# Kernel optimization log

Measured on AMD Instinct MI355X. Metric: run time of the kernel, lower is better.

## Reference

```python
import jax, jax.numpy as jnp
import numpy as np

EPS = 1e-8


def setup_inputs() -> dict:
    key = jax.random.key(0)
    kx, kw = jax.random.split(key)
    B, T, D_IN, D_OUT = 2, 2048, 4096, 16384
    x = jax.random.normal(kx, (B, T, D_IN), dtype=jnp.float32)
    # kaiming-uniform-ish scale for a (D_OUT, D_IN) linear weight
    bound = float(np.sqrt(6.0 / D_IN))
    weight = jax.random.uniform(kw, (D_OUT, D_IN), dtype=jnp.float32,
                                minval=-bound, maxval=bound)
    return {"x": x, "weight": weight}


def reference(x, weight):
    # --- ternary weight quantization (STE; value identical in train/eval) ---
    scale_w = jnp.mean(jnp.abs(weight))                       # scalar absmean
    w_q = jnp.clip(jnp.round(weight / (scale_w + EPS)), -1.0, 1.0) * scale_w
    w_quant = weight + jax.lax.stop_gradient(w_q - weight)    # STE

    # --- per-token INT8 activation quantization ---
    gamma = jnp.max(jnp.abs(x), axis=-1, keepdims=True)       # (B, T, 1)
    x_quant = jnp.clip(jnp.round(127.0 * x / (gamma + EPS)), -128.0, 127.0)
    scale_x = gamma / 127.0                                   # (B, T, 1)

    # --- GEMM + dequant epilogue ---
    out = jnp.einsum("btd,od->bto", x_quant, w_quant)         # (B, T, D_OUT)
    return out * scale_x
```

## Files before the change

kernel.cpp:

```cpp
#include <hip/hip_runtime.h>


#define M_ROWS 4096
#define K_DIM  4096
#define N_DIM  16384
#define W_ELEMS (N_DIM * K_DIM)
#define EPSF 1e-8f

using i32x4 = __attribute__((ext_vector_type(4))) int;


__global__ void k_abs_partial(const float4* __restrict__ w4,
                              double* __restrict__ part) {
    const int tid = threadIdx.x;
    int idx = blockIdx.x * 256 + tid;
    double s = 0.0;
    #pragma unroll 4
    for (int it = 0; it < 32; ++it) {
        float4 v = w4[idx + it * (2048 * 256)];
        s += (double)fabsf(v.x) + (double)fabsf(v.y)
           + (double)fabsf(v.z) + (double)fabsf(v.w);
    }
    __shared__ double red[256];
    red[tid] = s;
    __syncthreads();
    for (int o = 128; o > 0; o >>= 1) {
        if (tid < o) red[tid] += red[tid + o];
        __syncthreads();
    }
    if (tid == 0) part[blockIdx.x] = red[0];
}

__global__ void k_abs_final(const double* __restrict__ part,
                            float* __restrict__ scales) {
    const int tid = threadIdx.x;
    double s = 0.0;
    #pragma unroll
    for (int k = 0; k < 8; ++k) s += part[tid + k * 256];
    __shared__ double red[256];
    red[tid] = s;
    __syncthreads();
    for (int o = 128; o > 0; o >>= 1) {
        if (tid < o) red[tid] += red[tid + o];
        __syncthreads();
    }
    if (tid == 0) {
        float sw = (float)(red[0] / (double)W_ELEMS);
        scales[0] = sw;
        scales[1] = sw + EPSF;
    }
}

__global__ void k_wquant(const float4* __restrict__ w4,
                         const float* __restrict__ scales,
                         char4* __restrict__ wq4) {
    const float seps = scales[1];
    int idx = blockIdx.x * 256 + threadIdx.x;
    const int stride = 8192 * 256;
    #pragma unroll
    for (int it = 0; it < 8; ++it) {
        int i = idx + it * stride;
        float4 v = w4[i];
        char4 q;
        q.x = (signed char)(int)fminf(fmaxf(rintf(v.x / seps), -1.0f), 1.0f);
        q.y = (signed char)(int)fminf(fmaxf(rintf(v.y / seps), -1.0f), 1.0f);
        q.z = (signed char)(int)fminf(fmaxf(rintf(v.z / seps), -1.0f), 1.0f);
        q.w = (signed char)(int)fminf(fmaxf(rintf(v.w / seps), -1.0f), 1.0f);
        wq4[i] = q;
    }
}

__global__ void k_xquant(const float4* __restrict__ x4,
                         char4* __restrict__ xq4,
                         float* __restrict__ sx) {
    const int row = blockIdx.x, tid = threadIdx.x;
    const float4* xr = x4 + (size_t)row * (K_DIM / 4);
    float4 v[4];
    float m = 0.0f;
    #pragma unroll
    for (int j = 0; j < 4; ++j) {
        v[j] = xr[tid + j * 256];
        m = fmaxf(m, fmaxf(fmaxf(fabsf(v[j].x), fabsf(v[j].y)),
                           fmaxf(fabsf(v[j].z), fabsf(v[j].w))));
    }
    __shared__ float red[256];
    red[tid] = m;
    __syncthreads();
    for (int o = 128; o > 0; o >>= 1) {
        if (tid < o) red[tid] = fmaxf(red[tid], red[tid + o]);
        __syncthreads();
    }
    const float gamma = red[0];
    const float ge = gamma + EPSF;
    char4* out = xq4 + (size_t)row * (K_DIM / 4);
    #pragma unroll
    for (int j = 0; j < 4; ++j) {
        char4 q;
        q.x = (signed char)(int)fminf(fmaxf(rintf(127.0f * v[j].x / ge), -128.0f), 127.0f);
        q.y = (signed char)(int)fminf(fmaxf(rintf(127.0f * v[j].y / ge), -128.0f), 127.0f);
        q.z = (signed char)(int)fminf(fmaxf(rintf(127.0f * v[j].z / ge), -128.0f), 127.0f);
        q.w = (signed char)(int)fminf(fmaxf(rintf(127.0f * v[j].w / ge), -128.0f), 127.0f);
        out[tid + j * 256] = q;
    }
    if (tid == 0) sx[row] = gamma / 127.0f;
}

__device__ __forceinline__ void gload16(const signed char* g, const signed char* l) {
    __builtin_amdgcn_global_load_lds(
        (const __attribute__((address_space(1))) void*)g,
        (__attribute__((address_space(3))) void*)l, 16, 0, 0);
}

__global__ __launch_bounds__(256)
void k_gemm(const signed char* __restrict__ Aq,
            const signed char* __restrict__ Bq,
            const float* __restrict__ sx,
            const float* __restrict__ scales,
            float* __restrict__ C) {
    __shared__ __align__(16) signed char sA[128 * 64];
    __shared__ __align__(16) signed char sB[128 * 64];

    const int tid  = threadIdx.x;
    const int lane = tid & 63;
    const int wid  = tid >> 6;

    const int nwg = gridDim.x;
    const int cpx = nwg >> 3;
    const int bid = blockIdx.x;
    const int wg  = (bid & 7) * cpx + (bid >> 3);
    const int num_n = N_DIM / 128;
    const int per_group = 8 * num_n;
    const int gidx   = wg / per_group;
    const int within = wg - gidx * per_group;
    const int pm = gidx * 8 + (within & 7);
    const int pn = within >> 3;

    int prow[2], pcol[2], ldsoff[2];
    #pragma unroll
    for (int i = 0; i < 2; ++i) {
        int p = i * 4096 + tid * 16;
        int r = p >> 6;
        int j = (p >> 4) & 3;
        int js = j ^ ((r >> 1) & 3);
        prow[i]  = r;
        pcol[i]  = js << 4;
        ldsoff[i] = i * 4096 + wid * 1024;
    }
    const signed char* aSrc0 = Aq + (size_t)(pm * 128 + prow[0]) * K_DIM + pcol[0];
    const signed char* aSrc1 = Aq + (size_t)(pm * 128 + prow[1]) * K_DIM + pcol[1];
    const signed char* bSrc0 = Bq + (size_t)(pn * 128 + prow[0]) * K_DIM + pcol[0];
    const signed char* bSrc1 = Bq + (size_t)(pn * 128 + prow[1]) * K_DIM + pcol[1];

    const int wm  = (wid >> 1) * 64;
    const int wn  = (wid & 1) * 64;
    const int l15 = lane & 15;
    const int chunk = ((lane >> 4) ^ ((l15 >> 1) & 3)) << 4;

    i32x4 acc[4][4];
    #pragma unroll
    for (int a = 0; a < 4; ++a)
        #pragma unroll
        for (int b = 0; b < 4; ++b)
            acc[a][b] = (i32x4){0, 0, 0, 0};

    for (int kt = 0; kt < K_DIM / 64; ++kt) {
        const int ko = kt * 64;
        gload16(aSrc0 + ko, sA + ldsoff[0]);
        gload16(aSrc1 + ko, sA + ldsoff[1]);
        gload16(bSrc0 + ko, sB + ldsoff[0]);
        gload16(bSrc1 + ko, sB + ldsoff[1]);
        __syncthreads();

        i32x4 af[4], bf[4];
        #pragma unroll
        for (int f = 0; f < 4; ++f) {
            af[f] = *(const i32x4*)(sA + (wm + f * 16 + l15) * 64 + chunk);
            bf[f] = *(const i32x4*)(sB + (wn + f * 16 + l15) * 64 + chunk);
        }
        #pragma unroll
        for (int fm = 0; fm < 4; ++fm)
            #pragma unroll
            for (int fn = 0; fn < 4; ++fn)
                acc[fm][fn] = __builtin_amdgcn_mfma_i32_16x16x64_i8(
                    af[fm], bf[fn], acc[fm][fn], 0, 0, 0);
        __syncthreads();
    }

    const float sw = scales[0];
    const int gn0 = pn * 128 + wn + l15;
    const int gm_base = pm * 128 + wm + (lane >> 4) * 4;
    #pragma unroll
    for (int fm = 0; fm < 4; ++fm) {
        #pragma unroll
        for (int r = 0; r < 4; ++r) {
            const int gm = gm_base + fm * 16 + r;
            const float s = sx[gm] * sw;
            float* crow = C + (size_t)gm * N_DIM + gn0;
            #pragma unroll
            for (int fn = 0; fn < 4; ++fn)
                crow[fn * 16] = (float)acc[fm][fn][r] * s;
        }
    }
}

extern "C" void kernel_launch(void* const* d_in, const int* in_sizes, int n_in,
                              void* d_out, int out_size, void* d_ws, size_t ws_size,
                              hipStream_t stream) {
    const float* x = (const float*)d_in[0];
    const float* w = (const float*)d_in[1];
    float* out = (float*)d_out;
    char* ws = (char*)d_ws;

    float*  scales = (float*)(ws);
    double* part   = (double*)(ws + 1024);
    float*  sx     = (float*)(ws + 32 * 1024);
    signed char* xq = (signed char*)(ws + 64 * 1024);
    signed char* wq = xq + (size_t)M_ROWS * K_DIM;

    k_abs_partial<<<2048, 256, 0, stream>>>((const float4*)w, part);
    k_abs_final<<<1, 256, 0, stream>>>(part, scales);
    k_wquant<<<8192, 256, 0, stream>>>((const float4*)w, scales, (char4*)wq);
    k_xquant<<<M_ROWS, 256, 0, stream>>>((const float4*)x, (char4*)xq, sx);
    k_gemm<<<(M_ROWS / 128) * (N_DIM / 128), 256, 0, stream>>>(xq, wq, sx, scales, out);
}
```

Measured before the change: 500.4 us.

## Rewrite int8 GEMM as 256x256 tile, 8-wave, double-buffered pipelined kernel

Replaces the 128x128 single-buffered int8 MFMA GEMM with a 256x256 tile, 512-thread (8-wave) kernel that uses 128 KB of LDS as two buffers with K-step 128. Global-to-LDS loads for later K tiles are issued in quarter slices and interleaved with MFMA phases, using explicit vmcnt waits, barriers and raised wave priority around the math. An XOR swizzle avoids LDS bank conflicts. The aim is to hide global load latency and raise arithmetic intensity, at the cost of more registers (128 accumulators per thread) and a hand-tuned barrier schedule that is fragile to get right.

```diff
diff --git a/kernel.cpp b/kernel.cpp
--- a/kernel.cpp
+++ b/kernel.cpp
@@ -105,100 +105,151 @@
     if (tid == 0) sx[row] = gamma / 127.0f;
 }
 
-__device__ __forceinline__ void gload16(const signed char* g, const signed char* l) {
+__device__ __forceinline__ void gload16(const signed char* g, signed char* l) {
     __builtin_amdgcn_global_load_lds(
         (const __attribute__((address_space(1))) void*)g,
         (__attribute__((address_space(3))) void*)l, 16, 0, 0);
 }
 
-__global__ __launch_bounds__(256)
-void k_gemm(const signed char* __restrict__ Aq,
-            const signed char* __restrict__ Bq,
-            const float* __restrict__ sx,
-            const float* __restrict__ scales,
-            float* __restrict__ C) {
-    __shared__ __align__(16) signed char sA[128 * 64];
-    __shared__ __align__(16) signed char sB[128 * 64];
+#define BAR()   __builtin_amdgcn_s_barrier()
+#define LGKM0() asm volatile("s_waitcnt lgkmcnt(0)" ::: "memory")
+#define VM6()   asm volatile("s_waitcnt vmcnt(6)" ::: "memory")
+#define PRIO1() __builtin_amdgcn_s_setprio(1)
+#define PRIO0() __builtin_amdgcn_s_setprio(0)
+
+__global__ __launch_bounds__(512, 2)
+void k_gemm8(const signed char* __restrict__ Aq,
+             const signed char* __restrict__ Bq,
+             const float* __restrict__ sx,
+             const float* __restrict__ scales,
+             float* __restrict__ C) {
+    __shared__ __align__(16) signed char lds[131072];
 
     const int tid  = threadIdx.x;
     const int lane = tid & 63;
     const int wid  = tid >> 6;
-
-    const int nwg = gridDim.x;
-    const int cpx = nwg >> 3;
+    const int l15  = lane & 15;
+    const int qg   = lane >> 4;
+    const int swz  = l15 & 7;
+
     const int bid = blockIdx.x;
-    const int wg  = (bid & 7) * cpx + (bid >> 3);
-    const int num_n = N_DIM / 128;
-    const int per_group = 8 * num_n;
-    const int gidx   = wg / per_group;
-    const int within = wg - gidx * per_group;
+    const int wg  = (bid & 7) * 128 + (bid >> 3);
+    const int gidx   = wg >> 9;
+    const int within = wg & 511;
     const int pm = gidx * 8 + (within & 7);
     const int pn = within >> 3;
 
-    int prow[2], pcol[2], ldsoff[2];
-    #pragma unroll
-    for (int i = 0; i < 2; ++i) {
-        int p = i * 4096 + tid * 16;
-        int r = p >> 6;
-        int j = (p >> 4) & 3;
-        int js = j ^ ((r >> 1) & 3);
-        prow[i]  = r;
-        pcol[i]  = js << 4;
-        ldsoff[i] = i * 4096 + wid * 1024;
-    }
-    const signed char* aSrc0 = Aq + (size_t)(pm * 128 + prow[0]) * K_DIM + pcol[0];
-    const signed char* aSrc1 = Aq + (size_t)(pm * 128 + prow[1]) * K_DIM + pcol[1];
-    const signed char* bSrc0 = Bq + (size_t)(pn * 128 + prow[0]) * K_DIM + pcol[0];
-    const signed char* bSrc1 = Bq + (size_t)(pn * 128 + prow[1]) * K_DIM + pcol[1];
-
-    const int wm  = (wid >> 1) * 64;
-    const int wn  = (wid & 1) * 64;
-    const int l15 = lane & 15;
-    const int chunk = ((lane >> 4) ^ ((l15 >> 1) & 3)) << 4;
-
-    i32x4 acc[4][4];
-    #pragma unroll
-    for (int a = 0; a < 4; ++a)
+    const int wm = (wid >> 2) * 128;
+    const int wn = (wid & 3) * 64;
+
+    const int l3 = lane >> 3, l7 = lane & 7;
+    const int lane_off = l3 * K_DIM + ((l7 ^ l3) << 4);
+    const signed char* Asrc = Aq + (size_t)(pm * 256) * K_DIM + lane_off;
+    const signed char* Bsrc = Bq + (size_t)(pn * 256) * K_DIM + lane_off;
+    const int ar0 = wid * 8;
+    const int br0 = (wid >> 2) * 64 + (wid & 3) * 8;
+
+    auto stageA = [&](int buf, int mh, int kt) {
+        const int r0 = mh * 64 + ar0;
+        const signed char* s = Asrc + (size_t)r0 * K_DIM + kt * 128;
+        signed char* d = lds + buf * 65536 + r0 * 128;
+        gload16(s, d);
+        gload16(s + (size_t)128 * K_DIM, d + 128 * 128);
+    };
+    auto stageB = [&](int buf, int nh, int kt) {
+        const int r0 = nh * 32 + br0;
+        const signed char* s = Bsrc + (size_t)r0 * K_DIM + kt * 128;
+        signed char* d = lds + buf * 65536 + 32768 + r0 * 128;
+        gload16(s, d);
+        gload16(s + (size_t)128 * K_DIM, d + 128 * 128);
+    };
+
+    i32x4 acc[8][4];
+    #pragma unroll
+    for (int a = 0; a < 8; ++a)
         #pragma unroll
         for (int b = 0; b < 4; ++b)
             acc[a][b] = (i32x4){0, 0, 0, 0};
 
-    for (int kt = 0; kt < K_DIM / 64; ++kt) {
-        const int ko = kt * 64;
-        gload16(aSrc0 + ko, sA + ldsoff[0]);
-        gload16(aSrc1 + ko, sA + ldsoff[1]);
-        gload16(bSrc0 + ko, sB + ldsoff[0]);
-        gload16(bSrc1 + ko, sB + ldsoff[1]);
-        __syncthreads();
-
-        i32x4 af[4], bf[4];
-        #pragma unroll
-        for (int f = 0; f < 4; ++f) {
-            af[f] = *(const i32x4*)(sA + (wm + f * 16 + l15) * 64 + chunk);
-            bf[f] = *(const i32x4*)(sB + (wn + f * 16 + l15) * 64 + chunk);
+    i32x4 af[8], bf[4];
+    auto ldA = [&](int buf, int mh) {
+        const signed char* base = lds + buf * 65536;
+        #pragma unroll
+        for (int fm = 0; fm < 4; ++fm) {
+            const int ro = (wm + mh * 64 + fm * 16 + l15) * 128;
+            #pragma unroll
+            for (int ks = 0; ks < 2; ++ks)
+                af[fm * 2 + ks] = *(const i32x4*)(base + ro + (((ks * 4 + qg) ^ swz) << 4));
         }
-        #pragma unroll
-        for (int fm = 0; fm < 4; ++fm)
-            #pragma unroll
-            for (int fn = 0; fn < 4; ++fn)
-                acc[fm][fn] = __builtin_amdgcn_mfma_i32_16x16x64_i8(
-                    af[fm], bf[fn], acc[fm][fn], 0, 0, 0);
-        __syncthreads();
-    }
+    };
+    auto ldB = [&](int buf, int nh) {
+        const signed char* base = lds + buf * 65536 + 32768;
+        #pragma unroll
+        for (int fn = 0; fn < 2; ++fn) {
+            const int ro = (wn + nh * 32 + fn * 16 + l15) * 128;
+            #pragma unroll
+            for (int ks = 0; ks < 2; ++ks)
+                bf[fn * 2 + ks] = *(const i32x4*)(base + ro + (((ks * 4 + qg) ^ swz) << 4));
+        }
+    };
+    auto mma = [&](int mh, int nh) {
+        #pragma unroll
+        for (int ks = 0; ks < 2; ++ks)
+            #pragma unroll
+            for (int fm = 0; fm < 4; ++fm)
+                #pragma unroll
+                for (int fn = 0; fn < 2; ++fn)
+                    acc[mh * 4 + fm][nh * 2 + fn] = __builtin_amdgcn_mfma_i32_16x16x64_i8(
+                        af[fm * 2 + ks], bf[fn * 2 + ks], acc[mh * 4 + fm][nh * 2 + fn], 0, 0, 0);
+    };
+
+    stageA(0, 0, 0); stageB(0, 1, 0); stageA(0, 1, 0); stageB(0, 0, 0);
+    stageA(1, 0, 1); stageB(1, 1, 1); stageA(1, 1, 1);
+    VM6();
+    BAR();
+
+    for (int t = 0; t < 16; ++t) {
+        const int k1 = 2 * t + 1;
+        const int k2 = (2 * t + 2) & 31;
+        const int k3 = (2 * t + 3) & 31;
+
+        ldA(0, 0); ldB(0, 0); stageB(1, 0, k1);
+        BAR(); LGKM0(); PRIO1(); mma(0, 0); PRIO0(); BAR();
+        ldB(0, 1); stageA(0, 0, k2);
+        BAR(); LGKM0(); PRIO1(); mma(0, 1); PRIO0(); BAR();
+        ldA(0, 1); stageB(0, 1, k2);
+        BAR(); LGKM0(); PRIO1(); mma(1, 1); PRIO0(); BAR();
+        ldB(0, 0); stageA(0, 1, k2);
+        BAR(); LGKM0(); PRIO1(); mma(1, 0); PRIO0();
+        VM6();
+        BAR();
+        ldA(1, 0); ldB(1, 0); stageB(0, 0, k2);
+        BAR(); LGKM0(); PRIO1(); mma(0, 0); PRIO0(); BAR();
+        ldB(1, 1); stageA(1, 0, k3);
+        BAR(); LGKM0(); PRIO1(); mma(0, 1); PRIO0(); BAR();
+        ldA(1, 1); stageB(1, 1, k3);
+        BAR(); LGKM0(); PRIO1(); mma(1, 1); PRIO0(); BAR();
+        ldB(1, 0); stageA(1, 1, k3);
+        BAR(); LGKM0(); PRIO1(); mma(1, 0); PRIO0();
+        VM6();
+        BAR();
+    }
+    asm volatile("s_waitcnt vmcnt(0)" ::: "memory");
 
     const float sw = scales[0];
-    const int gn0 = pn * 128 + wn + l15;
-    const int gm_base = pm * 128 + wm + (lane >> 4) * 4;
-    #pragma unroll
-    for (int fm = 0; fm < 4; ++fm) {
+    const int gn0 = pn * 256 + wn + l15;
+    const int rb  = (lane >> 4) * 4;
+    #pragma unroll
+    for (int mi = 0; mi < 8; ++mi) {
+        const int rowoff = (mi >> 2) * 64 + (mi & 3) * 16;
         #pragma unroll
         for (int r = 0; r < 4; ++r) {
-            const int gm = gm_base + fm * 16 + r;
+            const int gm = pm * 256 + wm + rowoff + rb + r;
             const float s = sx[gm] * sw;
             float* crow = C + (size_t)gm * N_DIM + gn0;
             #pragma unroll
-            for (int fn = 0; fn < 4; ++fn)
-                crow[fn * 16] = (float)acc[fm][fn][r] * s;
+            for (int ni = 0; ni < 4; ++ni)
+                crow[(ni >> 1) * 32 + (ni & 1) * 16] = (float)acc[mi][ni][r] * s;
         }
     }
 }
@@ -221,5 +272,5 @@
     k_abs_final<<<1, 256, 0, stream>>>(part, scales);
     k_wquant<<<8192, 256, 0, stream>>>((const float4*)w, scales, (char4*)wq);
     k_xquant<<<M_ROWS, 256, 0, stream>>>((const float4*)x, (char4*)xq, sx);
-    k_gemm<<<(M_ROWS / 128) * (N_DIM / 128), 256, 0, stream>>>(xq, wq, sx, scales, out);
-}
+    k_gemm8<<<(M_ROWS / 256) * (N_DIM / 256), 512, 0, stream>>>(xq, wq, sx, scales, out);
+}
```

Measured after the change: 402.9 us. 19.5% less time.

## Rewrite int8 GEMM as 256x128 tile, 8-wave double-buffered pipelined kernel

Applied to the files above, without the earlier changes.

Replaces the 128x128, 4-wave GEMM with a 256x128 tile handled by 8 waves. It double-buffers LDS and splits each k-step into half-phases. Global-to-LDS loads for the next tiles are interleaved with MFMA work using s_waitcnt vmcnt(1), raw barriers, setprio and sched_barrier, and a new XOR swizzle layout is applied. The goal is to hide global load latency and cut per-k-step synchronisation stalls, at the cost of more LDS (48KB) and a delicate hand-written barrier schedule.

```diff
diff --git a/kernel.cpp b/kernel.cpp
--- a/kernel.cpp
+++ b/kernel.cpp
@@ -8,7 +8,6 @@
 #define EPSF 1e-8f
 
 using i32x4 = __attribute__((ext_vector_type(4))) int;
-
 
 __global__ void k_abs_partial(const float4* __restrict__ w4,
                               double* __restrict__ part) {
@@ -105,56 +104,58 @@
     if (tid == 0) sx[row] = gamma / 127.0f;
 }
 
-__device__ __forceinline__ void gload16(const signed char* g, const signed char* l) {
+__device__ __forceinline__ void gload16(const signed char* g, signed char* l) {
     __builtin_amdgcn_global_load_lds(
         (const __attribute__((address_space(1))) void*)g,
         (__attribute__((address_space(3))) void*)l, 16, 0, 0);
 }
 
-__global__ __launch_bounds__(256)
-void k_gemm(const signed char* __restrict__ Aq,
-            const signed char* __restrict__ Bq,
-            const float* __restrict__ sx,
-            const float* __restrict__ scales,
-            float* __restrict__ C) {
-    __shared__ __align__(16) signed char sA[128 * 64];
-    __shared__ __align__(16) signed char sB[128 * 64];
+#define BAR()   __builtin_amdgcn_s_barrier()
+#define VM1()   asm volatile("s_waitcnt vmcnt(1)" ::: "memory")
+#define PRIO1() __builtin_amdgcn_s_setprio(1)
+#define PRIO0() __builtin_amdgcn_s_setprio(0)
+#define SCHED0() __builtin_amdgcn_sched_barrier(0)
+
+__global__ __launch_bounds__(512, 4)
+void k_gemm8(const signed char* __restrict__ Aq,
+             const signed char* __restrict__ Bq,
+             const float* __restrict__ sx,
+             const float* __restrict__ scales,
+             float* __restrict__ C) {
+    __shared__ __align__(16) signed char lds[49152];
 
     const int tid  = threadIdx.x;
     const int lane = tid & 63;
     const int wid  = tid >> 6;
-
-    const int nwg = gridDim.x;
-    const int cpx = nwg >> 3;
+    const int l15  = lane & 15;
+    const int qg   = lane >> 4;
+
     const int bid = blockIdx.x;
-    const int wg  = (bid & 7) * cpx + (bid >> 3);
-    const int num_n = N_DIM / 128;
-    const int per_group = 8 * num_n;
-    const int gidx   = wg / per_group;
-    const int within = wg - gidx * per_group;
+    const int wg  = (bid & 7) * 256 + (bid >> 3);
+    const int gidx   = wg >> 10;
+    const int within = wg & 1023;
     const int pm = gidx * 8 + (within & 7);
     const int pn = within >> 3;
 
-    int prow[2], pcol[2], ldsoff[2];
-    #pragma unroll
-    for (int i = 0; i < 2; ++i) {
-        int p = i * 4096 + tid * 16;
-        int r = p >> 6;
-        int j = (p >> 4) & 3;
-        int js = j ^ ((r >> 1) & 3);
-        prow[i]  = r;
-        pcol[i]  = js << 4;
-        ldsoff[i] = i * 4096 + wid * 1024;
-    }
-    const signed char* aSrc0 = Aq + (size_t)(pm * 128 + prow[0]) * K_DIM + pcol[0];
-    const signed char* aSrc1 = Aq + (size_t)(pm * 128 + prow[1]) * K_DIM + pcol[1];
-    const signed char* bSrc0 = Bq + (size_t)(pn * 128 + prow[0]) * K_DIM + pcol[0];
-    const signed char* bSrc1 = Bq + (size_t)(pn * 128 + prow[1]) * K_DIM + pcol[1];
-
-    const int wm  = (wid >> 1) * 64;
-    const int wn  = (wid & 1) * 64;
-    const int l15 = lane & 15;
-    const int chunk = ((lane >> 4) ^ ((l15 >> 1) & 3)) << 4;
+    const int wm = (wid >> 1) * 64;
+    const int wn = (wid & 1) * 64;
+
+    const int srow  = tid >> 3;
+    const int slotd = (tid & 7) ^ (srow & 7);
+    const int relrow = 2 * srow + (slotd >> 2);
+    const int lane_off = relrow * K_DIM + (slotd & 3) * 16;
+    const signed char* Asrc = Aq + (size_t)(pm * 256) * K_DIM + lane_off;
+    const signed char* Bsrc = Bq + (size_t)(pn * 128) * K_DIM + lane_off;
+    signed char* const dA = lds + wid * 1024;
+    signed char* const dB = lds + 16384 + wid * 1024;
+
+    auto stageA = [&](int buf, int h, int kt) {
+        gload16(Asrc + (size_t)(h * 128) * K_DIM + kt * 64,
+                dA + buf * 24576 + h * 8192);
+    };
+    auto stageB = [&](int buf, int kt) {
+        gload16(Bsrc + kt * 64, dB + buf * 24576);
+    };
 
     i32x4 acc[4][4];
     #pragma unroll
@@ -163,37 +164,70 @@
         for (int b = 0; b < 4; ++b)
             acc[a][b] = (i32x4){0, 0, 0, 0};
 
-    for (int kt = 0; kt < K_DIM / 64; ++kt) {
-        const int ko = kt * 64;
-        gload16(aSrc0 + ko, sA + ldsoff[0]);
-        gload16(aSrc1 + ko, sA + ldsoff[1]);
-        gload16(bSrc0 + ko, sB + ldsoff[0]);
-        gload16(bSrc1 + ko, sB + ldsoff[1]);
-        __syncthreads();
-
-        i32x4 af[4], bf[4];
-        #pragma unroll
-        for (int f = 0; f < 4; ++f) {
-            af[f] = *(const i32x4*)(sA + (wm + f * 16 + l15) * 64 + chunk);
-            bf[f] = *(const i32x4*)(sB + (wn + f * 16 + l15) * 64 + chunk);
-        }
+    const int slotf = (((l15 & 1) << 2) + qg) ^ (l15 >> 1);
+    const int froff = (l15 >> 1) * 128 + slotf * 16;
+
+    i32x4 af[4], bf[4];
+    auto ldA = [&](int buf) {
+        const signed char* base = lds + buf * 24576 + wm * 64 + froff;
+        #pragma unroll
+        for (int fm = 0; fm < 4; ++fm)
+            af[fm] = *(const i32x4*)(base + fm * 1024);
+    };
+    auto ldB2 = [&](int buf, int half) {
+        const signed char* base = lds + buf * 24576 + 16384 + wn * 64 + froff;
+        #pragma unroll
+        for (int f = 0; f < 2; ++f)
+            bf[half * 2 + f] = *(const i32x4*)(base + (half * 2 + f) * 1024);
+    };
+    auto mma2 = [&](int half) {
         #pragma unroll
         for (int fm = 0; fm < 4; ++fm)
             #pragma unroll
-            for (int fn = 0; fn < 4; ++fn)
-                acc[fm][fn] = __builtin_amdgcn_mfma_i32_16x16x64_i8(
-                    af[fm], bf[fn], acc[fm][fn], 0, 0, 0);
-        __syncthreads();
-    }
+            for (int f = 0; f < 2; ++f)
+                acc[fm][half * 2 + f] = __builtin_amdgcn_mfma_i32_16x16x64_i8(
+                    af[fm], bf[half * 2 + f], acc[fm][half * 2 + f], 0, 0, 0);
+    };
+
+    stageA(0, 0, 0); stageA(0, 1, 0); stageB(0, 0);
+    stageA(1, 0, 1);
+    VM1();
+    BAR();
+
+    for (int t = 0; t < 32; ++t) {
+        const int k1 = 2 * t + 1;
+        const int k2 = (2 * t + 2) & 63;
+        const int k3 = (2 * t + 3) & 63;
+
+        ldA(0); ldB2(0, 0);
+        stageA(1, 1, k1); stageB(1, k1);
+        BAR(); PRIO1(); mma2(0); PRIO0(); SCHED0();
+        ldB2(0, 1); SCHED0();
+        BAR();
+        stageA(0, 0, k2);
+        BAR(); PRIO1(); mma2(1); PRIO0(); SCHED0();
+        VM1();
+        BAR();
+        ldA(1); ldB2(1, 0);
+        stageA(0, 1, k2); stageB(0, k2);
+        BAR(); PRIO1(); mma2(0); PRIO0(); SCHED0();
+        ldB2(1, 1); SCHED0();
+        BAR();
+        stageA(1, 0, k3);
+        BAR(); PRIO1(); mma2(1); PRIO0(); SCHED0();
+        VM1();
+        BAR();
+    }
+    asm volatile("s_waitcnt vmcnt(0)" ::: "memory");
 
     const float sw = scales[0];
     const int gn0 = pn * 128 + wn + l15;
-    const int gm_base = pm * 128 + wm + (lane >> 4) * 4;
+    const int rb  = qg * 4;
     #pragma unroll
     for (int fm = 0; fm < 4; ++fm) {
         #pragma unroll
         for (int r = 0; r < 4; ++r) {
-            const int gm = gm_base + fm * 16 + r;
+            const int gm = pm * 256 + wm + fm * 16 + rb + r;
             const float s = sx[gm] * sw;
             float* crow = C + (size_t)gm * N_DIM + gn0;
             #pragma unroll
@@ -221,5 +255,5 @@
     k_abs_final<<<1, 256, 0, stream>>>(part, scales);
     k_wquant<<<8192, 256, 0, stream>>>((const float4*)w, scales, (char4*)wq);
     k_xquant<<<M_ROWS, 256, 0, stream>>>((const float4*)x, (char4*)xq, sx);
-    k_gemm<<<(M_ROWS / 128) * (N_DIM / 128), 256, 0, stream>>>(xq, wq, sx, scales, out);
-}
+    k_gemm8<<<(M_ROWS / 256) * (N_DIM / 128), 512, 0, stream>>>(xq, wq, sx, scales, out);
+}
```

Result: faster. 468.2 us (-6.4%).
